# Kernel tuning notes

Hardware: AMD Instinct MI355X
Metric: run time of the kernel (lower is better)

Reference implementation:

```python
import jax, jax.numpy as jnp
import numpy as np

D = 128          # in_dim
B = 64           # graphs in batch
NP = 625         # nodes per graph
N = B * NP       # 40000 nodes
EH = 200000      # directed edges per direction
E = 2 * EH       # 400000 symmetric edges
THRESH = 0.0
CC_ITERS = 20
LN_EPS = 1e-5


def setup_inputs() -> dict:
    rng = np.random.default_rng(0)
    g = rng.integers(0, B, EH)
    src = (g * NP + rng.integers(0, NP, EH)).astype(np.int32)
    dst = (g * NP + rng.integers(0, NP, EH)).astype(np.int32)
    edge_index = np.stack([np.concatenate([src, dst]), np.concatenate([dst, src])])
    rev_idx = np.concatenate([np.arange(EH) + EH, np.arange(EH)]).astype(np.int32)
    batch = np.repeat(np.arange(B), NP).astype(np.int32)
    key = jax.random.key(0)
    ks = jax.random.split(key, 16)
    lin = lambda k, o, i: jax.random.normal(k, (o, i), jnp.float32) / np.sqrt(i)
    return dict(
        x=jax.random.normal(ks[0], (N, D), jnp.float32),
        edge_attr=jax.random.normal(ks[1], (E, D), jnp.float32),
        query=jax.random.normal(ks[2], (B, D), jnp.float32),
        qW=lin(ks[3], D, D), qb=jnp.zeros((D,), jnp.float32),
        kW=lin(ks[4], D, D), kb=jnp.zeros((D,), jnp.float32),
        vW=lin(ks[5], D, D), vb=jnp.zeros((D,), jnp.float32),
        prelu_a=jnp.array(0.25, jnp.float32),
        ln_g=jnp.ones((D,), jnp.float32), ln_b=jnp.zeros((D,), jnp.float32),
        attnW=lin(ks[6], 1, D),
        g1W=lin(ks[7], D, D), g1b=jnp.zeros((D,), jnp.float32),
        g2W=lin(ks[8], D, D), g2b=jnp.zeros((D,), jnp.float32),
        edge_index=jnp.asarray(edge_index),
        batch=jnp.asarray(batch),
        rev_idx=jnp.asarray(rev_idx),
    )


def _seg_mean(v, ids, n):
    s = jax.ops.segment_sum(v, ids, num_segments=n)
    c = jax.ops.segment_sum(jnp.ones(ids.shape, jnp.float32), ids, num_segments=n)
    c = jnp.maximum(c, 1.0)
    return s / (c[:, None] if v.ndim > 1 else c)


def reference(x, edge_attr, query, qW, qb, kW, kb, vW, vb, prelu_a, ln_g, ln_b,
              attnW, g1W, g1b, g2W, g2b, edge_index, batch, rev_idx):
    row, col = edge_index[0], edge_index[1]
    edge_batch = batch[row]
    # edge -> node scatter-mean, gathered back to edges and mixed with x[row]
    msg = _seg_mean(edge_attr, col, N)
    ea = (edge_attr + msg[row] + x[row]) / 3.0
    unit = 0.5 * (ea + ea[rev_idx])              # to_undirected(reduce='mean')
    V = ea @ vW.T + vb
    K = unit @ kW.T + kb
    Q = (query @ qW.T + qb)[edge_batch]
    score = jnp.sum(K * Q, -1) / (jnp.linalg.norm(Q, axis=-1) * jnp.linalg.norm(K, axis=-1))
    score = jnp.tanh(score)                      # score_act (threshold mode)
    mean_s = _seg_mean(score, edge_batch, B)[edge_batch]
    perm = (score < mean_s) & (score <= THRESH)  # edges selected for contraction
    # edge features gated by score, PReLU + LayerNorm
    ea2 = V * score[:, None]
    ea2 = jnp.where(ea2 >= 0, ea2, prelu_a * ea2)
    mu = ea2.mean(-1, keepdims=True)
    var = ea2.var(-1, keepdims=True)
    ea2 = (ea2 - mu) * jax.lax.rsqrt(var + LN_EPS) * ln_g + ln_b
    # clustering: connected components over 'perm' edges (min-label prop + pointer jumping)
    big = jnp.int32(N)
    def body(i, lab):
        lr = jnp.where(perm, lab[row], big)
        lc = jnp.where(perm, lab[col], big)
        new = lab.at[row].min(lc).at[col].min(lr)
        new = jnp.minimum(new, lab)
        new = new[new]
        return new[new]
    comp = jax.lax.fori_loop(0, CC_ITERS, body, jnp.arange(N, dtype=jnp.int32))
    # GINE conv (eps=0, MLP d->d->d) over contracted edges only
    m = jnp.where(perm[:, None], jax.nn.relu(x[row] + ea2), 0.0)
    agg = jax.ops.segment_sum(m, col, num_segments=N)
    h = x + agg
    x_sparse = jax.nn.relu(h @ g1W.T + g1b) @ g2W.T + g2b
    # per-component attention softmax pooling
    logit = jax.nn.leaky_relu(x_sparse @ attnW.T)[:, 0]
    mx = jax.ops.segment_max(logit, comp, num_segments=N)
    ex = jnp.exp(logit - mx[comp])
    den = jax.ops.segment_sum(ex, comp, num_segments=N)
    attn = ex / den[comp]
    x_out = jax.ops.segment_sum(attn[:, None] * x_sparse, comp, num_segments=N)
    # edge_reduce (drop intra-cluster) + coalesce (sort keys, segment-sum attrs), padded to E
    rc, cc = comp[row], comp[col]
    valid = rc != cc
    keyv = jnp.where(valid, rc.astype(jnp.int64) * N + cc, jnp.int64(N) * N)
    order = jnp.argsort(keyv)
    ksort = keyv[order]
    seg = jnp.cumsum(jnp.concatenate([jnp.zeros((1,), jnp.int32),
                                      (ksort[1:] != ksort[:-1]).astype(jnp.int32)]))
    ea_sorted = jnp.where(valid[order][:, None], ea2[order], 0.0)
    edge_attr_out = jax.ops.segment_sum(ea_sorted, seg, num_segments=E)
    row_out = jax.ops.segment_max(jnp.where(valid, rc, -1)[order], seg, num_segments=E)
    col_out = jax.ops.segment_max(jnp.where(valid, cc, -1)[order], seg, num_segments=E)
    edge_index_out = jnp.stack([row_out, col_out])
    return x_out, edge_index_out, edge_attr_out, score
```

## Files before the change

kernel.cpp:

```cpp
#include <hip/hip_runtime.h>
#include <math.h>
#include <stdint.h>

#define D 128
#define NG 64
#define NP 625
#define NN 40000
#define NE 400000
#define EH 200000
#define CCIT 20
#define KPG (NP*NP)
#define NKEY (NG*KPG)
#define NWORD (NKEY/32)
#define SCANB ((NWORD+255)/256)
#define NBLKN ((NN+255)/256)
#define LN_EPSF 1e-5f

#define ROW_OFF   ((size_t)NN*D)
#define COL_OFF   (ROW_OFF + NE)
#define EAOUT_OFF (COL_OFF + NE)
#define SCORE_OFF (EAOUT_OFF + (size_t)NE*D)
#define OUT_TOTAL (SCORE_OFF + NE)

typedef __attribute__((ext_vector_type(8))) short bf16x8;
typedef __attribute__((ext_vector_type(4))) float f32x4;
typedef __attribute__((ext_vector_type(4))) unsigned uint4v;

__device__ __forceinline__ unsigned fenc(float f) {
  unsigned u = __float_as_uint(f);
  return (u & 0x80000000u) ? ~u : (u | 0x80000000u);
}
__device__ __forceinline__ float fdec(unsigned u) {
  return (u & 0x80000000u) ? __uint_as_float(u & 0x7FFFFFFFu) : __uint_as_float(~u);
}

__device__ __forceinline__ void split8(float4 a, float4 b, bf16x8& hi, bf16x8& lo) {
  const float v[8] = {a.x, a.y, a.z, a.w, b.x, b.y, b.z, b.w};
  uint4v H, L;
#pragma unroll
  for (int p = 0; p < 4; p++) {
    unsigned u0 = __float_as_uint(v[2*p]);
    unsigned u1 = __float_as_uint(v[2*p + 1]);
    unsigned r0 = (u0 + 0x8000u) & 0xFFFF0000u;
    unsigned r1 = (u1 + 0x8000u) & 0xFFFF0000u;
    float l0 = v[2*p]     - __uint_as_float(r0);
    float l1 = v[2*p + 1] - __uint_as_float(r1);
    H[p] = (r0 >> 16) | r1;
    L[p] = (__float_as_uint(l0) >> 16) | (__float_as_uint(l1) & 0xFFFF0000u);
  }
  hi = __builtin_bit_cast(bf16x8, H);
  lo = __builtin_bit_cast(bf16x8, L);
}

__device__ __forceinline__ void mm8l(const float* __restrict__ wq,
                                     const float* __restrict__ wb,
                                     int lane,
                                     float* __restrict__ a0,
                                     float* __restrict__ a1) {
  const float4* wq4 = (const float4*)wq;
  const float4* b4  = (const float4*)wb;
#pragma unroll 2
  for (int dq = 0; dq < 16; dq++) {
    float4 wA = wq4[dq*128 + lane];
    float4 wB = wq4[dq*128 + lane + 64];
    float4 wC = wq4[(dq+16)*128 + lane];
    float4 wD = wq4[(dq+16)*128 + lane + 64];
#pragma unroll
    for (int t = 0; t < 8; t++) {
      float4 bL = b4[t*32 + dq];
      float4 bH = b4[t*32 + 16 + dq];
#pragma unroll
      for (int k = 0; k < 4; k++) {
        a0[t] += (&bL.x)[k]*(&wA.x)[k] + (&bH.x)[k]*(&wC.x)[k];
        a1[t] += (&bL.x)[k]*(&wB.x)[k] + (&bH.x)[k]*(&wD.x)[k];
      }
    }
  }
}

__global__ void k_transp(const float* __restrict__ kW, float* __restrict__ wTk) {
  int i = blockIdx.x*blockDim.x + threadIdx.x;
  int d = i & 127, j = i >> 7;
  wTk[(((d >> 2)*128 + j) << 2) + (d & 3)] = kW[j*D + d];
}

__global__ void k_packw(const float* __restrict__ vW, const float* __restrict__ g1W,
                        const float* __restrict__ g2W,
                        unsigned short* __restrict__ pvh, unsigned short* __restrict__ pvl,
                        unsigned short* __restrict__ p1h, unsigned short* __restrict__ p1l,
                        unsigned short* __restrict__ p2h, unsigned short* __restrict__ p2l) {
  int t = blockIdx.x*blockDim.x + threadIdx.x;
  if (t >= 3*2048) return;
  int w = t >> 11, idx = t & 2047;
  int f = idx >> 6, l = idx & 63;
  int n = f >> 2, ks = f & 3;
  int j = n*16 + (l & 15);
  int d0 = ks*32 + (l >> 4)*8;
  const float* W = (w == 0) ? vW : (w == 1) ? g1W : g2W;
  unsigned short* ph = (w == 0) ? pvh : (w == 1) ? p1h : p2h;
  unsigned short* pl = (w == 0) ? pvl : (w == 1) ? p1l : p2l;
#pragma unroll
  for (int i = 0; i < 8; i++) {
    float x = W[j*D + d0 + i];
    unsigned u = __float_as_uint(x);
    unsigned rh = (u + 0x7FFFu + ((u >> 16) & 1u)) & 0xFFFF0000u;
    float lf = x - __uint_as_float(rh);
    unsigned ul = __float_as_uint(lf);
    unsigned rl = (ul + 0x7FFFu + ((ul >> 16) & 1u)) >> 16;
    ph[(size_t)(f*64 + l)*8 + i] = (unsigned short)(rh >> 16);
    pl[(size_t)(f*64 + l)*8 + i] = (unsigned short)rl;
  }
}

__global__ void k_init(unsigned* __restrict__ mx, float* __restrict__ out) {
  int i = blockIdx.x*blockDim.x + threadIdx.x;
  int n = blockDim.x*gridDim.x;
  for (int k = i; k < NN; k += n) mx[k] = 0x007FFFFFu;
  for (int k = i; k < 2*NE; k += n) out[ROW_OFF + k] = -2147483648.0f;
}

__global__ __launch_bounds__(128) void k_qmat(
    const float* __restrict__ query, const float* __restrict__ qW,
    const float* __restrict__ qb, float* __restrict__ Qm, float* __restrict__ qn) {
  int g = blockIdx.x, j = threadIdx.x;
  __shared__ float qs[D];
  __shared__ float red[D];
  qs[j] = query[g*D + j];
  __syncthreads();
  float acc = qb[j];
  for (int d = 0; d < D; d++) acc += qs[d]*qW[j*D + d];
  Qm[g*D + j] = acc;
  red[j] = acc*acc;
  __syncthreads();
  for (int off = 64; off > 0; off >>= 1) {
    if (j < off) red[j] += red[j+off];
    __syncthreads();
  }
  if (j == 0) qn[g] = sqrtf(red[0]);
}

__global__ void k_count(const int* __restrict__ ei, int* __restrict__ cnt) {
  int stride = blockDim.x*gridDim.x;
  for (int e = blockIdx.x*blockDim.x + threadIdx.x; e < NE; e += stride) {
    atomicAdd(&cnt[ei[NE + e]], 1);
  }
}

__global__ __launch_bounds__(256) void k_scanA(
    const int* __restrict__ cnt, int* __restrict__ start, int* __restrict__ bsumN) {
  __shared__ int buf[256];
  int i = blockIdx.x*256 + threadIdx.x;
  int v = (i < NN) ? cnt[i] : 0;
  buf[threadIdx.x] = v;
  __syncthreads();
  for (int o = 1; o < 256; o <<= 1) {
    int x = (threadIdx.x >= o) ? buf[threadIdx.x - o] : 0;
    __syncthreads();
    buf[threadIdx.x] += x;
    __syncthreads();
  }
  if (i < NN) start[i] = buf[threadIdx.x] - v;
  if (threadIdx.x == 255) bsumN[blockIdx.x] = buf[255];
}

__global__ __launch_bounds__(256) void k_scanB(int* __restrict__ bsumN) {
  __shared__ int buf[256];
  int t = threadIdx.x;
  int v = (t < NBLKN) ? bsumN[t] : 0;
  buf[t] = v;
  __syncthreads();
  for (int o = 1; o < 256; o <<= 1) {
    int x = (t >= o) ? buf[t-o] : 0;
    __syncthreads();
    buf[t] += x;
    __syncthreads();
  }
  if (t < NBLKN) bsumN[t] = buf[t] - v;
}

__global__ __launch_bounds__(256) void k_scanC(
    int* __restrict__ start, const int* __restrict__ bsumN) {
  int i = blockIdx.x*256 + threadIdx.x;
  if (i < NN) start[i] += bsumN[blockIdx.x];
  if (i == 0) start[NN] = NE;
}

__global__ void k_fillcsr(const int* __restrict__ ei,
                          int* __restrict__ fillc, const int* __restrict__ start,
                          int* __restrict__ csr) {
  int stride = blockDim.x*gridDim.x;
  for (int e = blockIdx.x*blockDim.x + threadIdx.x; e < NE; e += stride) {
    int c = ei[NE + e];
    int s = atomicAdd(&fillc[c], 1);
    csr[start[c] + s] = e;
  }
}

__global__ void k_sortcsr(const int* __restrict__ start, int* __restrict__ csr) {
  int n = blockIdx.x*blockDim.x + threadIdx.x;
  if (n >= NN) return;
  int a = start[n], b = start[n+1];
  for (int i = a+1; i < b; i++) {
    int v = csr[i]; int k = i-1;
    while (k >= a && csr[k] > v) { csr[k+1] = csr[k]; k--; }
    csr[k+1] = v;
  }
}

__global__ void k_msg(const float* __restrict__ edge_attr, const int* __restrict__ start,
                      const int* __restrict__ csr, float* __restrict__ msg) {
  int wid = (blockIdx.x*blockDim.x + threadIdx.x) >> 6;
  int lane = threadIdx.x & 63;
  if (wid >= NN) return;
  int a = start[wid], b = start[wid+1];
  float s0 = 0.f, s1 = 0.f;
  for (int k = a; k < b; k++) {
    const float* p = edge_attr + (size_t)csr[k]*D;
    s0 += p[lane]; s1 += p[lane+64];
  }
  float c = (float)max(b-a, 1);
  msg[(size_t)wid*D + lane]      = s0/c;
  msg[(size_t)wid*D + lane + 64] = s1/c;
}

__global__ void k_ea(const float* __restrict__ edge_attr, const float* __restrict__ msg,
                     const float* __restrict__ x, const int* __restrict__ ei,
                     float* __restrict__ ea) {
  size_t stride = (size_t)blockDim.x*gridDim.x;
  size_t total = (size_t)NE*(D/4);
  for (size_t i = (size_t)blockIdx.x*blockDim.x + threadIdx.x; i < total; i += stride) {
    size_t e = i >> 5;
    int q = (int)(i & 31);
    int r = ei[e];
    float4 A = ((const float4*)(edge_attr + e*D))[q];
    float4 M = ((const float4*)(msg + (size_t)r*D))[q];
    float4 X = ((const float4*)(x + (size_t)r*D))[q];
    float4 o;
    o.x = (A.x + M.x + X.x) / 3.0f;
    o.y = (A.y + M.y + X.y) / 3.0f;
    o.z = (A.z + M.z + X.z) / 3.0f;
    o.w = (A.w + M.w + X.w) / 3.0f;
    ((float4*)(ea + e*D))[q] = o;
  }
}

__global__ __launch_bounds__(256) void k_score(
    const float* __restrict__ ea,
    const int* __restrict__ ei, const int* __restrict__ batch,
    const float* __restrict__ wqk, const float* __restrict__ kb,
    const float* __restrict__ Qm, const float* __restrict__ qn,
    float* __restrict__ score_out) {
  __shared__ float sbuf[4][8*D];
  float* wb = sbuf[threadIdx.x >> 6];
  const int lane = threadIdx.x & 63;
  const int wid = (blockIdx.x*256 + threadIdx.x) >> 6;
  const int nw = (gridDim.x*256) >> 6;
  const float kb0 = kb[lane], kb1 = kb[lane+64];
  for (int base = wid*8; base < EH; base += nw*8) {
    float a0[8], a1[8];
#pragma unroll
    for (int t = 0; t < 8; t++) {
      int e = base + t;
      const float* pe = ea + (size_t)e*D;
      const float* pr = ea + (size_t)(e + EH)*D;
      wb[t*D + lane]      = 0.5f*(pe[lane]    + pr[lane]);
      wb[t*D + lane + 64] = 0.5f*(pe[lane+64] + pr[lane+64]);
      a0[t] = kb0; a1[t] = kb1;
    }
    mm8l(wqk, wb, lane, a0, a1);
#pragma unroll
    for (int t = 0; t < 8; t++) {
      int e = base + t;
      int g = batch[ei[e]];
      float q0 = Qm[g*D + lane], q1 = Qm[g*D + lane + 64];
      float p  = a0[t]*q0 + a1[t]*q1;
      float nk = a0[t]*a0[t] + a1[t]*a1[t];
#pragma unroll
      for (int off = 32; off > 0; off >>= 1) {
        p  += __shfl_xor(p,  off, 64);
        nk += __shfl_xor(nk, off, 64);
      }
      if (lane == 0) {
        float s = p / (qn[g] * sqrtf(nk));
        float sv = tanhf(s);
        score_out[e] = sv;
        score_out[e + EH] = sv;
      }
    }
  }
}

__global__ __launch_bounds__(256) void k_mean(
    const float* __restrict__ score, const int* __restrict__ start,
    const int* __restrict__ csr, float* __restrict__ gmean) {
  int g = blockIdx.x;
  int a = start[g*NP], b = start[(g+1)*NP];
  double s = 0.0;
  for (int k = a + threadIdx.x; k < b; k += blockDim.x) s += (double)score[csr[k]];
  __shared__ double red[256];
  red[threadIdx.x] = s;
  __syncthreads();
  for (int off = 128; off > 0; off >>= 1) {
    if (threadIdx.x < off) red[threadIdx.x] += red[threadIdx.x + off];
    __syncthreads();
  }
  if (threadIdx.x == 0) gmean[g] = (float)(red[0] / (double)max(b - a, 1));
}

__global__ __launch_bounds__(256) void k_vea2m(
    float* __restrict__ ea, const float* __restrict__ score,
    const int* __restrict__ ei, const int* __restrict__ batch,
    const unsigned short* __restrict__ whi, const unsigned short* __restrict__ wlo,
    const float* __restrict__ vb, const float* __restrict__ prelu_a,
    const float* __restrict__ ln_g, const float* __restrict__ ln_b,
    const float* __restrict__ gmean, unsigned char* __restrict__ perm) {
  const int wid = (blockIdx.x*256 + threadIdx.x) >> 6;
  const int lane = threadIdx.x & 63;
  if (wid >= NE/32) return;
  const int rbase = wid*32;
  const int lg = lane >> 4, lm = lane & 15;
  float vb8[8], lg8[8], lb8[8];
#pragma unroll
  for (int n = 0; n < 8; n++) {
    vb8[n] = vb[lm + 16*n];
    lg8[n] = ln_g[lm + 16*n];
    lb8[n] = ln_b[lm + 16*n];
  }
  f32x4 acc[2][8];
#pragma unroll
  for (int m = 0; m < 2; m++)
#pragma unroll
    for (int n = 0; n < 8; n++) {
      acc[m][n][0] = vb8[n]; acc[m][n][1] = vb8[n];
      acc[m][n][2] = vb8[n]; acc[m][n][3] = vb8[n];
    }
#pragma unroll
  for (int ks = 0; ks < 4; ks++) {
    bf16x8 ahi[2], alo[2];
#pragma unroll
    for (int m = 0; m < 2; m++) {
      const float* p = ea + (size_t)(rbase + m*16 + lm)*D + ks*32 + lg*8;
      float4 x0 = ((const float4*)p)[0];
      float4 x1 = ((const float4*)p)[1];
      split8(x0, x1, ahi[m], alo[m]);
    }
#pragma unroll
    for (int n = 0; n < 8; n++) {
      const bf16x8 bhi = *(const bf16x8*)(whi + ((size_t)(n*4 + ks)*64 + lane)*8);
      const bf16x8 blo = *(const bf16x8*)(wlo + ((size_t)(n*4 + ks)*64 + lane)*8);
#pragma unroll
      for (int m = 0; m < 2; m++) {
        acc[m][n] = __builtin_amdgcn_mfma_f32_16x16x32_bf16(ahi[m], bhi, acc[m][n], 0, 0, 0);
        acc[m][n] = __builtin_amdgcn_mfma_f32_16x16x32_bf16(ahi[m], blo, acc[m][n], 0, 0, 0);
        acc[m][n] = __builtin_amdgcn_mfma_f32_16x16x32_bf16(alo[m], bhi, acc[m][n], 0, 0, 0);
      }
    }
  }
  const float pa = prelu_a[0];
#pragma unroll
  for (int m = 0; m < 2; m++) {
#pragma unroll
    for (int r = 0; r < 4; r++) {
      const int e = rbase + m*16 + lg*4 + r;
      const float s = score[e];
      float y[8];
      float tot = 0.f;
#pragma unroll
      for (int n = 0; n < 8; n++) {
        float v = acc[m][n][r] * s;
        v = (v >= 0.f) ? v : pa*v;
        y[n] = v;
        tot += v;
      }
#pragma unroll
      for (int off = 8; off > 0; off >>= 1) tot += __shfl_xor(tot, off, 64);
      const float mu = tot * (1.0f/128.0f);
      float sq = 0.f;
#pragma unroll
      for (int n = 0; n < 8; n++) { y[n] -= mu; sq += y[n]*y[n]; }
#pragma unroll
      for (int off = 8; off > 0; off >>= 1) sq += __shfl_xor(sq, off, 64);
      const float inv = rsqrtf(sq*(1.0f/128.0f) + LN_EPSF);
      float* po = ea + (size_t)e*D + lm;
#pragma unroll
      for (int n = 0; n < 8; n++) po[16*n] = y[n]*inv*lg8[n] + lb8[n];
      if (lm == 0) {
        const int g = batch[ei[e]];
        perm[e] = (unsigned char)((s < gmean[g]) && (s <= 0.0f));
      }
    }
  }
}

__global__ __launch_bounds__(256) void k_cc(
    const int* __restrict__ ei, const unsigned char* __restrict__ perm,
    const int* __restrict__ start, const int* __restrict__ csr,
    int* __restrict__ comp) {
  __shared__ unsigned short er[8192], ec[8192];
  __shared__ int lab[NP], tmp[NP];
  __shared__ int cnt;
  int g = blockIdx.x;
  int base = g*NP;
  if (threadIdx.x == 0) cnt = 0;
  for (int i = threadIdx.x; i < NP; i += blockDim.x) lab[i] = i;
  __syncthreads();
  int a = start[base], b = start[base + NP];
  for (int k = a + threadIdx.x; k < b; k += blockDim.x) {
    int e = csr[k];
    if (perm[e]) {
      int idx = atomicAdd(&cnt, 1);
      if (idx < 8192) {
        er[idx] = (unsigned short)(ei[e] - base);
        ec[idx] = (unsigned short)(ei[NE + e] - base);
      }
    }
  }
  __syncthreads();
  int m = min(cnt, 8192);
  for (int it = 0; it < CCIT; it++) {
    for (int k = threadIdx.x; k < m; k += blockDim.x) {
      int r = er[k], c = ec[k];
      atomicMin(&lab[r], lab[c]);
      atomicMin(&lab[c], lab[r]);
    }
    __syncthreads();
    for (int i = threadIdx.x; i < NP; i += blockDim.x) tmp[i] = lab[lab[i]];
    __syncthreads();
    for (int i = threadIdx.x; i < NP; i += blockDim.x) lab[i] = tmp[tmp[i]];
    __syncthreads();
  }
  for (int i = threadIdx.x; i < NP; i += blockDim.x) comp[base + i] = base + lab[i];
}

__global__ void k_gine(const float* __restrict__ x, const float* __restrict__ ea2,
                       const int* __restrict__ ei, const unsigned char* __restrict__ perm,
                       const int* __restrict__ start, const int* __restrict__ csr,
                       float* __restrict__ h) {
  int wid = (blockIdx.x*blockDim.x + threadIdx.x) >> 6;
  int lane = threadIdx.x & 63;
  if (wid >= NN) return;
  int a = start[wid], b = start[wid+1];
  float s0 = 0.f, s1 = 0.f;
  for (int k = a; k < b; k++) {
    int e = csr[k];
    if (!perm[e]) continue;
    int r = ei[e];
    const float* pe = ea2 + (size_t)e*D;
    const float* px = x + (size_t)r*D;
    s0 += fmaxf(px[lane]      + pe[lane],      0.f);
    s1 += fmaxf(px[lane + 64] + pe[lane + 64], 0.f);
  }
  h[(size_t)wid*D + lane]      = x[(size_t)wid*D + lane]      + s0;
  h[(size_t)wid*D + lane + 64] = x[(size_t)wid*D + lane + 64] + s1;
}

__global__ __launch_bounds__(256) void k_rowmm_m(
    const float* __restrict__ in, const unsigned short* __restrict__ whi,
    const unsigned short* __restrict__ wlo, const float* __restrict__ bias,
    float* __restrict__ out, int ntile32, int do_relu) {
  const int wid = (blockIdx.x*256 + threadIdx.x) >> 6;
  const int lane = threadIdx.x & 63;
  if (wid >= ntile32) return;
  const int rbase = wid*32;
  const int lg = lane >> 4, lm = lane & 15;
  float b8[8];
#pragma unroll
  for (int n = 0; n < 8; n++) b8[n] = bias[lm + 16*n];
  f32x4 acc[2][8];
#pragma unroll
  for (int m = 0; m < 2; m++)
#pragma unroll
    for (int n = 0; n < 8; n++) {
      acc[m][n][0] = b8[n]; acc[m][n][1] = b8[n];
      acc[m][n][2] = b8[n]; acc[m][n][3] = b8[n];
    }
#pragma unroll
  for (int ks = 0; ks < 4; ks++) {
    bf16x8 ahi[2], alo[2];
#pragma unroll
    for (int m = 0; m < 2; m++) {
      const float* p = in + (size_t)(rbase + m*16 + lm)*D + ks*32 + lg*8;
      float4 x0 = ((const float4*)p)[0];
      float4 x1 = ((const float4*)p)[1];
      split8(x0, x1, ahi[m], alo[m]);
    }
#pragma unroll
    for (int n = 0; n < 8; n++) {
      const bf16x8 bhi = *(const bf16x8*)(whi + ((size_t)(n*4 + ks)*64 + lane)*8);
      const bf16x8 blo = *(const bf16x8*)(wlo + ((size_t)(n*4 + ks)*64 + lane)*8);
#pragma unroll
      for (int m = 0; m < 2; m++) {
        acc[m][n] = __builtin_amdgcn_mfma_f32_16x16x32_bf16(ahi[m], bhi, acc[m][n], 0, 0, 0);
        acc[m][n] = __builtin_amdgcn_mfma_f32_16x16x32_bf16(ahi[m], blo, acc[m][n], 0, 0, 0);
        acc[m][n] = __builtin_amdgcn_mfma_f32_16x16x32_bf16(alo[m], bhi, acc[m][n], 0, 0, 0);
      }
    }
  }
#pragma unroll
  for (int m = 0; m < 2; m++) {
#pragma unroll
    for (int r = 0; r < 4; r++) {
      const int row = rbase + m*16 + lg*4 + r;
      float* po = out + (size_t)row*D + lm;
#pragma unroll
      for (int n = 0; n < 8; n++) {
        float v = acc[m][n][r];
        if (do_relu) v = fmaxf(v, 0.f);
        po[16*n] = v;
      }
    }
  }
}

__global__ void k_logit(const float* __restrict__ xs, const float* __restrict__ attnW,
                        const int* __restrict__ comp, float* __restrict__ logit,
                        unsigned* __restrict__ mx) {
  int wid = (blockIdx.x*blockDim.x + threadIdx.x) >> 6;
  int lane = threadIdx.x & 63;
  if (wid >= NN) return;
  float p = xs[(size_t)wid*D + lane]*attnW[lane] + xs[(size_t)wid*D + lane + 64]*attnW[lane + 64];
#pragma unroll
  for (int off = 32; off > 0; off >>= 1) p += __shfl_xor(p, off, 64);
  if (lane == 0) {
    float l = (p >= 0.f) ? p : 0.01f*p;
    logit[wid] = l;
    atomicMax(&mx[comp[wid]], fenc(l));
  }
}

__global__ void k_expden(const float* __restrict__ logit, const int* __restrict__ comp,
                         const unsigned* __restrict__ mx, float* __restrict__ exv,
                         float* __restrict__ den) {
  int n = blockIdx.x*blockDim.x + threadIdx.x;
  if (n >= NN) return;
  float m = fdec(mx[comp[n]]);
  float e = expf(logit[n] - m);
  exv[n] = e;
  atomicAdd(&den[comp[n]], e);
}

__global__ void k_pool(const float* __restrict__ xs, const float* __restrict__ exv,
                       const float* __restrict__ den, const int* __restrict__ comp,
                       float* __restrict__ xout) {
  int wid = (blockIdx.x*blockDim.x + threadIdx.x) >> 6;
  int lane = threadIdx.x & 63;
  if (wid >= NN) return;
  float w = exv[wid] / den[comp[wid]];
  size_t dst = (size_t)comp[wid]*D;
  atomicAdd(&xout[dst + lane],      w*xs[(size_t)wid*D + lane]);
  atomicAdd(&xout[dst + lane + 64], w*xs[(size_t)wid*D + lane + 64]);
}

__global__ void k_bitmap(const int* __restrict__ ei, const int* __restrict__ comp,
                         const int* __restrict__ batch, unsigned* __restrict__ bitmap,
                         int* __restrict__ validcnt) {
  __shared__ int lv;
  if (threadIdx.x == 0) lv = 0;
  __syncthreads();
  int stride = blockDim.x*gridDim.x;
  for (int e = blockIdx.x*blockDim.x + threadIdx.x; e < NE; e += stride) {
    int r = ei[e], c = ei[NE + e];
    int rc = comp[r], cc = comp[c];
    if (rc != cc) {
      int g = batch[r];
      int lr = rc - g*NP, lc = cc - g*NP;
      if ((unsigned)lr < NP && (unsigned)lc < NP) {
        int ck = g*KPG + lr*NP + lc;
        atomicOr(&bitmap[ck >> 5], 1u << (ck & 31));
        atomicAdd(&lv, 1);
      }
    }
  }
  __syncthreads();
  if (threadIdx.x == 0) atomicAdd(validcnt, lv);
}

__global__ __launch_bounds__(256) void k_scan1(const unsigned* __restrict__ bitmap,
                                               unsigned* __restrict__ wpref,
                                               unsigned* __restrict__ bsum) {
  __shared__ unsigned buf[256];
  int i = blockIdx.x*256 + threadIdx.x;
  unsigned v = (i < NWORD) ? (unsigned)__popc(bitmap[i]) : 0u;
  buf[threadIdx.x] = v;
  __syncthreads();
  for (int o = 1; o < 256; o <<= 1) {
    unsigned x = (threadIdx.x >= o) ? buf[threadIdx.x - o] : 0u;
    __syncthreads();
    buf[threadIdx.x] += x;
    __syncthreads();
  }
  if (i < NWORD) wpref[i] = buf[threadIdx.x] - v;
  if (threadIdx.x == 255) bsum[blockIdx.x] = buf[255];
}

__global__ __launch_bounds__(256) void k_scan2(unsigned* __restrict__ bsum,
                                               int* __restrict__ U) {
  __shared__ unsigned buf[256];
  __shared__ unsigned carry;
  int t = threadIdx.x;
  if (t == 0) carry = 0;
  __syncthreads();
  for (int base = 0; base < SCANB; base += 256) {
    int i = base + t;
    unsigned v = (i < SCANB) ? bsum[i] : 0u;
    buf[t] = v; __syncthreads();
    for (int o = 1; o < 256; o <<= 1) {
      unsigned x = (t >= o) ? buf[t-o] : 0u;
      __syncthreads();
      buf[t] += x;
      __syncthreads();
    }
    if (i < SCANB) bsum[i] = carry + buf[t] - v;
    unsigned tot = buf[255];
    __syncthreads();
    if (t == 0) carry += tot;
    __syncthreads();
  }
  if (t == 0) *U = (int)carry;
}

__global__ void k_scan3(unsigned* __restrict__ wpref, const unsigned* __restrict__ bsum) {
  int i = blockIdx.x*256 + threadIdx.x;
  if (i < NWORD) wpref[i] += bsum[blockIdx.x];
}

__global__ void k_coalesce(const int* __restrict__ ei, const int* __restrict__ comp,
                           const int* __restrict__ batch, const float* __restrict__ ea2,
                           const unsigned* __restrict__ bitmap, const unsigned* __restrict__ wpref,
                           float* __restrict__ out) {
  const int lane = threadIdx.x & 63;
  int wid = (blockIdx.x*blockDim.x + threadIdx.x) >> 6;
  int nw = (gridDim.x*blockDim.x) >> 6;
  for (int e = wid; e < NE; e += nw) {
    int r = ei[e], c = ei[NE + e];
    int rc = comp[r], cc = comp[c];
    if (rc == cc) continue;
    int g = batch[r];
    int lr = rc - g*NP, lc = cc - g*NP;
    if ((unsigned)lr >= NP || (unsigned)lc >= NP) continue;
    int ck = g*KPG + lr*NP + lc;
    int wd = ck >> 5, bit = ck & 31;
    unsigned rank = wpref[wd] + (unsigned)__popc(bitmap[wd] & ((1u << bit) - 1u));
    const float* pe = ea2 + (size_t)e*D;
    float* po = out + EAOUT_OFF + (size_t)rank*D;
    atomicAdd(&po[lane],      pe[lane]);
    atomicAdd(&po[lane + 64], pe[lane + 64]);
    if (lane == 0) {
      out[ROW_OFF + rank] = (float)rc;
      out[COL_OFF + rank] = (float)cc;
    }
  }
}

__global__ void k_tail(const int* __restrict__ U, const int* __restrict__ validcnt,
                       float* __restrict__ out) {
  if (blockIdx.x == 0 && threadIdx.x == 0) {
    int u = *U;
    if (*validcnt < NE && u < NE) {
      out[ROW_OFF + u] = -1.0f;
      out[COL_OFF + u] = -1.0f;
    }
  }
}

extern "C" void kernel_launch(void* const* d_in, const int* in_sizes, int n_in,
                              void* d_out, int out_size, void* d_ws, size_t ws_size,
                              hipStream_t stream) {
  const float* x         = (const float*)d_in[0];
  const float* edge_attr = (const float*)d_in[1];
  const float* query     = (const float*)d_in[2];
  const float* qW = (const float*)d_in[3];
  const float* qb = (const float*)d_in[4];
  const float* kW = (const float*)d_in[5];
  const float* kb = (const float*)d_in[6];
  const float* vW = (const float*)d_in[7];
  const float* vb = (const float*)d_in[8];
  const float* prelu_a = (const float*)d_in[9];
  const float* ln_g = (const float*)d_in[10];
  const float* ln_b = (const float*)d_in[11];
  const float* attnW = (const float*)d_in[12];
  const float* g1W = (const float*)d_in[13];
  const float* g1b = (const float*)d_in[14];
  const float* g2W = (const float*)d_in[15];
  const float* g2b = (const float*)d_in[16];
  const int* ei    = (const int*)d_in[17];
  const int* batch = (const int*)d_in[18];
  const int* rev   = (const int*)d_in[19];
  float* out = (float*)d_out;
  (void)in_sizes; (void)n_in; (void)out_size; (void)rev;

  char* w = (char*)d_ws;
  size_t off = 0;
  auto alloc = [&](size_t bytes) -> void* {
    void* p = w + off;
    off = (off + bytes + 255) & ~(size_t)255;
    return p;
  };
  float* ea = (float*)alloc((size_t)NE*D*4);
  float* h  = (float*)alloc((size_t)NN*D*4);
  float* t1 = (float*)alloc((size_t)NN*D*4);
  float* xs = (float*)alloc((size_t)NN*D*4);
  float* Qm = (float*)alloc((size_t)NG*D*4);
  float* qn = (float*)alloc(NG*4);
  float* gmean = (float*)alloc(NG*4);
  float* wTk = (float*)alloc((size_t)D*D*4);
  unsigned short* pvh = (unsigned short*)alloc((size_t)D*D*2);
  unsigned short* pvl = (unsigned short*)alloc((size_t)D*D*2);
  unsigned short* p1h = (unsigned short*)alloc((size_t)D*D*2);
  unsigned short* p1l = (unsigned short*)alloc((size_t)D*D*2);
  unsigned short* p2h = (unsigned short*)alloc((size_t)D*D*2);
  unsigned short* p2l = (unsigned short*)alloc((size_t)D*D*2);
  int* comp   = (int*)alloc((size_t)NN*4);
  float* logit = (float*)alloc((size_t)NN*4);
  float* exv   = (float*)alloc((size_t)NN*4);
  int* startc = (int*)alloc((size_t)(NN+1)*4);
  int* csr    = (int*)alloc((size_t)NE*4);
  unsigned char* perm = (unsigned char*)alloc(NE);
  unsigned* wpref = (unsigned*)alloc((size_t)NWORD*4);
  unsigned* bsum  = (unsigned*)alloc((size_t)(SCANB+32)*4);
  int* bsumN = (int*)alloc((size_t)(NBLKN+32)*4);
  int* Uv = (int*)alloc(256);
  unsigned* mx = (unsigned*)alloc((size_t)NN*4);
  size_t z0 = off;
  int* cnt   = (int*)alloc((size_t)NN*4);
  int* fillc = (int*)alloc((size_t)NN*4);
  float* den = (float*)alloc((size_t)NN*4);
  int* validcnt = (int*)alloc(256);
  unsigned* bitmap = (unsigned*)alloc((size_t)NWORD*4);
  size_t z1 = off;
  if (off > ws_size) return;

  hipMemsetAsync(d_out, 0, OUT_TOTAL*4, stream);
  hipMemsetAsync(w + z0, 0, z1 - z0, stream);

  k_transp<<<64, 256, 0, stream>>>(kW, wTk);
  k_packw<<<24, 256, 0, stream>>>(vW, g1W, g2W, pvh, pvl, p1h, p1l, p2h, p2l);
  k_init<<<1024, 256, 0, stream>>>(mx, out);
  k_qmat<<<NG, 128, 0, stream>>>(query, qW, qb, Qm, qn);
  k_count<<<512, 256, 0, stream>>>(ei, cnt);
  k_scanA<<<NBLKN, 256, 0, stream>>>(cnt, startc, bsumN);
  k_scanB<<<1, 256, 0, stream>>>(bsumN);
  k_scanC<<<NBLKN, 256, 0, stream>>>(startc, bsumN);
  k_fillcsr<<<512, 256, 0, stream>>>(ei, fillc, startc, csr);
  k_sortcsr<<<(NN+255)/256, 256, 0, stream>>>(startc, csr);
  k_msg<<<NN/4, 256, 0, stream>>>(edge_attr, startc, csr, h);
  k_ea<<<8192, 256, 0, stream>>>(edge_attr, h, x, ei, ea);
  k_score<<<2048, 256, 0, stream>>>(ea, ei, batch, wTk, kb, Qm, qn, out + SCORE_OFF);
  k_mean<<<NG, 256, 0, stream>>>(out + SCORE_OFF, startc, csr, gmean);
  k_vea2m<<<(NE/32 + 3)/4, 256, 0, stream>>>(ea, out + SCORE_OFF, ei, batch,
                                             pvh, pvl, vb, prelu_a, ln_g, ln_b,
                                             gmean, perm);
  k_cc<<<NG, 256, 0, stream>>>(ei, perm, startc, csr, comp);
  k_gine<<<NN/4, 256, 0, stream>>>(x, ea, ei, perm, startc, csr, h);
  k_rowmm_m<<<(NN/32 + 3)/4, 256, 0, stream>>>(h, p1h, p1l, g1b, t1, NN/32, 1);
  k_rowmm_m<<<(NN/32 + 3)/4, 256, 0, stream>>>(t1, p2h, p2l, g2b, xs, NN/32, 0);
  k_logit<<<NN/4, 256, 0, stream>>>(xs, attnW, comp, logit, mx);
  k_expden<<<(NN+255)/256, 256, 0, stream>>>(logit, comp, mx, exv, den);
  k_pool<<<NN/4, 256, 0, stream>>>(xs, exv, den, comp, out);
  k_bitmap<<<512, 256, 0, stream>>>(ei, comp, batch, bitmap, validcnt);
  k_scan1<<<SCANB, 256, 0, stream>>>(bitmap, wpref, bsum);
  k_scan2<<<1, 256, 0, stream>>>(bsum, Uv);
  k_scan3<<<SCANB, 256, 0, stream>>>(wpref, bsum);
  k_coalesce<<<2048, 256, 0, stream>>>(ei, comp, batch, ea, bitmap, wpref, out);
  k_tail<<<1, 64, 0, stream>>>(Uv, validcnt, out);
}
```

Before: 1.380 ms.

## Compute edge scores with split-bf16 MFMA and repair near-threshold edges in fp32

Replaces the scalar fp32 key-projection score kernel with an MFMA kernel that uses a hi/lo bf16 split of both the edge features and the packed kW weights. To guard the threshold decisions against rounding, it flags edges whose score lies within a small margin of the graph mean or of zero. Those edges are recomputed with the original fp32 path. This adds two small kernels and a capped suspect list, and relies on the margin being wide enough to cover the split-bf16 error.

```diff
diff --git a/kernel.cpp b/kernel.cpp
--- a/kernel.cpp
+++ b/kernel.cpp
@@ -15,6 +15,9 @@
 #define SCANB ((NWORD+255)/256)
 #define NBLKN ((NN+255)/256)
 #define LN_EPSF 1e-5f
+#define SCT (EH/32)
+#define SUSCAP 65536
+#define MARG 3e-4f
 
 #define ROW_OFF   ((size_t)NN*D)
 #define COL_OFF   (ROW_OFF + NE)
@@ -85,20 +88,21 @@
 }
 
 __global__ void k_packw(const float* __restrict__ vW, const float* __restrict__ g1W,
-                        const float* __restrict__ g2W,
+                        const float* __restrict__ g2W, const float* __restrict__ kW,
                         unsigned short* __restrict__ pvh, unsigned short* __restrict__ pvl,
                         unsigned short* __restrict__ p1h, unsigned short* __restrict__ p1l,
-                        unsigned short* __restrict__ p2h, unsigned short* __restrict__ p2l) {
+                        unsigned short* __restrict__ p2h, unsigned short* __restrict__ p2l,
+                        unsigned short* __restrict__ pkh, unsigned short* __restrict__ pkl) {
   int t = blockIdx.x*blockDim.x + threadIdx.x;
-  if (t >= 3*2048) return;
+  if (t >= 4*2048) return;
   int w = t >> 11, idx = t & 2047;
   int f = idx >> 6, l = idx & 63;
   int n = f >> 2, ks = f & 3;
   int j = n*16 + (l & 15);
   int d0 = ks*32 + (l >> 4)*8;
-  const float* W = (w == 0) ? vW : (w == 1) ? g1W : g2W;
-  unsigned short* ph = (w == 0) ? pvh : (w == 1) ? p1h : p2h;
-  unsigned short* pl = (w == 0) ? pvl : (w == 1) ? p1l : p2l;
+  const float* W = (w == 0) ? vW : (w == 1) ? g1W : (w == 2) ? g2W : kW;
+  unsigned short* ph = (w == 0) ? pvh : (w == 1) ? p1h : (w == 2) ? p2h : pkh;
+  unsigned short* pl = (w == 0) ? pvl : (w == 1) ? p1l : (w == 2) ? p2l : pkl;
 #pragma unroll
   for (int i = 0; i < 8; i++) {
     float x = W[j*D + d0 + i];
@@ -244,8 +248,121 @@
   }
 }
 
-__global__ __launch_bounds__(256) void k_score(
+__global__ __launch_bounds__(256) void k_scoreM(
     const float* __restrict__ ea,
+    const int* __restrict__ ei, const int* __restrict__ batch,
+    const unsigned short* __restrict__ whi, const unsigned short* __restrict__ wlo,
+    const float* __restrict__ kb, const float* __restrict__ Qm,
+    const float* __restrict__ qn, float* __restrict__ score_out) {
+  const int wid = (blockIdx.x*256 + threadIdx.x) >> 6;
+  const int lane = threadIdx.x & 63;
+  if (wid >= SCT) return;
+  const int rbase = wid*32;
+  const int lg = lane >> 4, lm = lane & 15;
+  float kb8[8];
+#pragma unroll
+  for (int n = 0; n < 8; n++) kb8[n] = kb[lm + 16*n];
+  f32x4 acc[2][8];
+#pragma unroll
+  for (int m = 0; m < 2; m++)
+#pragma unroll
+    for (int n = 0; n < 8; n++) {
+      acc[m][n][0] = kb8[n]; acc[m][n][1] = kb8[n];
+      acc[m][n][2] = kb8[n]; acc[m][n][3] = kb8[n];
+    }
+#pragma unroll
+  for (int ks = 0; ks < 4; ks++) {
+    bf16x8 ahi[2], alo[2];
+#pragma unroll
+    for (int m = 0; m < 2; m++) {
+      const float* p  = ea + (size_t)(rbase + m*16 + lm)*D + ks*32 + lg*8;
+      const float* pr = p + (size_t)EH*D;
+      float4 e0 = ((const float4*)p)[0];
+      float4 e1 = ((const float4*)p)[1];
+      float4 r0 = ((const float4*)pr)[0];
+      float4 r1 = ((const float4*)pr)[1];
+      float4 x0, x1;
+      x0.x = 0.5f*(e0.x + r0.x); x0.y = 0.5f*(e0.y + r0.y);
+      x0.z = 0.5f*(e0.z + r0.z); x0.w = 0.5f*(e0.w + r0.w);
+      x1.x = 0.5f*(e1.x + r1.x); x1.y = 0.5f*(e1.y + r1.y);
+      x1.z = 0.5f*(e1.z + r1.z); x1.w = 0.5f*(e1.w + r1.w);
+      split8(x0, x1, ahi[m], alo[m]);
+    }
+#pragma unroll
+    for (int n = 0; n < 8; n++) {
+      const bf16x8 bhi = *(const bf16x8*)(whi + ((size_t)(n*4 + ks)*64 + lane)*8);
+      const bf16x8 blo = *(const bf16x8*)(wlo + ((size_t)(n*4 + ks)*64 + lane)*8);
+#pragma unroll
+      for (int m = 0; m < 2; m++) {
+        acc[m][n] = __builtin_amdgcn_mfma_f32_16x16x32_bf16(ahi[m], bhi, acc[m][n], 0, 0, 0);
+        acc[m][n] = __builtin_amdgcn_mfma_f32_16x16x32_bf16(ahi[m], blo, acc[m][n], 0, 0, 0);
+        acc[m][n] = __builtin_amdgcn_mfma_f32_16x16x32_bf16(alo[m], bhi, acc[m][n], 0, 0, 0);
+        acc[m][n] = __builtin_amdgcn_mfma_f32_16x16x32_bf16(alo[m], blo, acc[m][n], 0, 0, 0);
+      }
+    }
+  }
+#pragma unroll
+  for (int m = 0; m < 2; m++) {
+#pragma unroll
+    for (int r = 0; r < 4; r++) {
+      const int e = rbase + m*16 + lg*4 + r;
+      const int g = batch[ei[e]];
+      float p = 0.f, nk = 0.f;
+#pragma unroll
+      for (int n = 0; n < 8; n++) {
+        float kv = acc[m][n][r];
+        p  += kv * Qm[g*D + lm + 16*n];
+        nk += kv * kv;
+      }
+#pragma unroll
+      for (int off = 8; off > 0; off >>= 1) {
+        p  += __shfl_xor(p,  off, 64);
+        nk += __shfl_xor(nk, off, 64);
+      }
+      float s = p / (qn[g] * sqrtf(nk));
+      float sv = tanhf(s);
+      if (lm == 0) {
+        score_out[e] = sv;
+        score_out[e + EH] = sv;
+      }
+    }
+  }
+}
+
+__global__ __launch_bounds__(256) void k_mean(
+    const float* __restrict__ score, const int* __restrict__ start,
+    const int* __restrict__ csr, float* __restrict__ gmean) {
+  int g = blockIdx.x;
+  int a = start[g*NP], b = start[(g+1)*NP];
+  double s = 0.0;
+  for (int k = a + threadIdx.x; k < b; k += blockDim.x) s += (double)score[csr[k]];
+  __shared__ double red[256];
+  red[threadIdx.x] = s;
+  __syncthreads();
+  for (int off = 128; off > 0; off >>= 1) {
+    if (threadIdx.x < off) red[threadIdx.x] += red[threadIdx.x + off];
+    __syncthreads();
+  }
+  if (threadIdx.x == 0) gmean[g] = (float)(red[0] / (double)max(b - a, 1));
+}
+
+__global__ void k_suspect(const float* __restrict__ score, const int* __restrict__ ei,
+                          const int* __restrict__ batch, const float* __restrict__ gmean,
+                          int* __restrict__ list, int* __restrict__ nsus) {
+  int e = blockIdx.x*blockDim.x + threadIdx.x;
+  if (e >= EH) return;
+  float s = score[e];
+  int g = batch[ei[e]];
+  float gm = gmean[g];
+  if (fabsf(s - gm) < MARG || fabsf(s) < MARG) {
+    int i = atomicAdd(nsus, 1);
+    if (i < SUSCAP) list[i] = e;
+  }
+}
+
+__global__ __launch_bounds__(256) void k_repair(
+    const float* __restrict__ ea, const int* __restrict__ list,
+    const int* __restrict__ nsus_p,
     const int* __restrict__ ei, const int* __restrict__ batch,
     const float* __restrict__ wqk, const float* __restrict__ kb,
     const float* __restrict__ Qm, const float* __restrict__ qn,
@@ -255,12 +372,16 @@
   const int lane = threadIdx.x & 63;
   const int wid = (blockIdx.x*256 + threadIdx.x) >> 6;
   const int nw = (gridDim.x*256) >> 6;
+  const int nsus = min(*nsus_p, SUSCAP);
   const float kb0 = kb[lane], kb1 = kb[lane+64];
-  for (int base = wid*8; base < EH; base += nw*8) {
+  for (int base = wid*8; base < nsus; base += nw*8) {
     float a0[8], a1[8];
+    int el[8];
 #pragma unroll
     for (int t = 0; t < 8; t++) {
-      int e = base + t;
+      int idx = base + t;
+      int e = (idx < nsus) ? list[idx] : list[base];
+      el[t] = (idx < nsus) ? e : -1;
       const float* pe = ea + (size_t)e*D;
       const float* pr = ea + (size_t)(e + EH)*D;
       wb[t*D + lane]      = 0.5f*(pe[lane]    + pr[lane]);
@@ -270,7 +391,8 @@
     mm8l(wqk, wb, lane, a0, a1);
 #pragma unroll
     for (int t = 0; t < 8; t++) {
-      int e = base + t;
+      if (el[t] < 0) continue;
+      int e = el[t];
       int g = batch[ei[e]];
       float q0 = Qm[g*D + lane], q1 = Qm[g*D + lane + 64];
       float p  = a0[t]*q0 + a1[t]*q1;
@@ -288,23 +410,6 @@
       }
     }
   }
-}
-
-__global__ __launch_bounds__(256) void k_mean(
-    const float* __restrict__ score, const int* __restrict__ start,
-    const int* __restrict__ csr, float* __restrict__ gmean) {
-  int g = blockIdx.x;
-  int a = start[g*NP], b = start[(g+1)*NP];
-  double s = 0.0;
-  for (int k = a + threadIdx.x; k < b; k += blockDim.x) s += (double)score[csr[k]];
-  __shared__ double red[256];
-  red[threadIdx.x] = s;
-  __syncthreads();
-  for (int off = 128; off > 0; off >>= 1) {
-    if (threadIdx.x < off) red[threadIdx.x] += red[threadIdx.x + off];
-    __syncthreads();
-  }
-  if (threadIdx.x == 0) gmean[g] = (float)(red[0] / (double)max(b - a, 1));
 }
 
 __global__ __launch_bounds__(256) void k_vea2m(
@@ -710,6 +815,9 @@
   unsigned short* p1l = (unsigned short*)alloc((size_t)D*D*2);
   unsigned short* p2h = (unsigned short*)alloc((size_t)D*D*2);
   unsigned short* p2l = (unsigned short*)alloc((size_t)D*D*2);
+  unsigned short* pkh = (unsigned short*)alloc((size_t)D*D*2);
+  unsigned short* pkl = (unsigned short*)alloc((size_t)D*D*2);
+  int* suslist = (int*)alloc((size_t)SUSCAP*4);
   int* comp   = (int*)alloc((size_t)NN*4);
   float* logit = (float*)alloc((size_t)NN*4);
   float* exv   = (float*)alloc((size_t)NN*4);
@@ -726,6 +834,7 @@
   int* fillc = (int*)alloc((size_t)NN*4);
   float* den = (float*)alloc((size_t)NN*4);
   int* validcnt = (int*)alloc(256);
+  int* nsus = (int*)alloc(256);
   unsigned* bitmap = (unsigned*)alloc((size_t)NWORD*4);
   size_t z1 = off;
   if (off > ws_size) return;
@@ -734,7 +843,8 @@
   hipMemsetAsync(w + z0, 0, z1 - z0, stream);
 
   k_transp<<<64, 256, 0, stream>>>(kW, wTk);
-  k_packw<<<24, 256, 0, stream>>>(vW, g1W, g2W, pvh, pvl, p1h, p1l, p2h, p2l);
+  k_packw<<<32, 256, 0, stream>>>(vW, g1W, g2W, kW, pvh, pvl, p1h, p1l,
+                                  p2h, p2l, pkh, pkl);
   k_init<<<1024, 256, 0, stream>>>(mx, out);
   k_qmat<<<NG, 128, 0, stream>>>(query, qW, qb, Qm, qn);
   k_count<<<512, 256, 0, stream>>>(ei, cnt);
@@ -745,8 +855,13 @@
   k_sortcsr<<<(NN+255)/256, 256, 0, stream>>>(startc, csr);
   k_msg<<<NN/4, 256, 0, stream>>>(edge_attr, startc, csr, h);
   k_ea<<<8192, 256, 0, stream>>>(edge_attr, h, x, ei, ea);
-  k_score<<<2048, 256, 0, stream>>>(ea, ei, batch, wTk, kb, Qm, qn, out + SCORE_OFF);
+  k_scoreM<<<(SCT + 3)/4, 256, 0, stream>>>(ea, ei, batch, pkh, pkl, kb, Qm, qn,
+                                            out + SCORE_OFF);
   k_mean<<<NG, 256, 0, stream>>>(out + SCORE_OFF, startc, csr, gmean);
+  k_suspect<<<(EH+255)/256, 256, 0, stream>>>(out + SCORE_OFF, ei, batch, gmean,
+                                              suslist, nsus);
+  k_repair<<<64, 256, 0, stream>>>(ea, suslist, nsus, ei, batch, wTk, kb, Qm, qn,
+                                   out + SCORE_OFF);
   k_vea2m<<<(NE/32 + 3)/4, 256, 0, stream>>>(ea, out + SCORE_OFF, ei, batch,
                                              pvh, pvl, vb, prelu_a, ln_g, ln_b,
                                              gmean, perm);
```

Result: faster. 1.321 ms (-4.2%).
